# Kernel tuning notes

Measured on AMD Instinct MI355X. Metric: run time of the kernel, lower is better.

The kernel has to match this reference:

```python
import jax, jax.numpy as jnp
import numpy as np

EPS = 1e-7

def _dubbed_squash(v):
    norm = jnp.linalg.norm(v, axis=-1, keepdims=True)
    coef = 1.0 - 1.0 / (jnp.exp(norm) + EPS)
    return coef * v / (norm + EPS)

def setup_inputs() -> dict:
    key = jax.random.key(0)
    k1, k2, k3 = jax.random.split(key, 3)
    B, N, dp = 16, 1152, 8   # batch, num_primary_caps, dim_primary_caps
    D, dd = 10, 16           # num_digit_caps, dim_digit_caps
    primary_caps = jax.random.normal(k1, (B, N, dp), dtype=jnp.float32)
    W = jax.random.normal(k2, (D, N, dd, dp), dtype=jnp.float32) * 0.05
    B_prior = jax.random.normal(k3, (D, 1, N), dtype=jnp.float32) * 0.05
    return {"primary_caps": primary_caps, "W": W, "B_prior": B_prior}

def reference(primary_caps, W, B_prior):
    dp = primary_caps.shape[-1]
    # votes: U_hat[b,d,n,j] = W[d,n,j,i] @ u[b,n,i]   (replaces the tf.map_fn)
    U_hat = jnp.einsum('dnji,bni->bdnj', W, primary_caps)  # [B,D,N,dd]
    # self-similarity score matrix (as in original: full NxN matmul)
    A = jnp.einsum('bdnj,bdmj->bdnm', U_hat, U_hat) / jnp.sqrt(
        jnp.asarray(dp, dtype=primary_caps.dtype))          # [B,D,N,N]
    A_sum = jnp.sum(A, axis=2, keepdims=True)               # [B,D,1,N]
    C = jax.nn.softmax(A_sum, axis=1)                       # softmax over digit axis
    # weighted combine with learned log-priors: (B+C) @ U_hat -> [B,D,1,dd] -> squeeze
    S = jnp.einsum('bdkn,bdnj->bdj', B_prior[None] + C, U_hat)  # [B,D,dd]
    return _dubbed_squash(S)
```

## Files before the change

### kernel.cpp

```cpp
#include <hip/hip_runtime.h>

constexpr int BN = 16, NN = 1152, DP = 8, ND = 10, DD = 16;
constexpr int NBLK = BN * ND;
constexpr int GG = 64;
constexpr int KPT = NN / GG;
constexpr unsigned MAG1 = 0xC0FFEE01u;
constexpr int SPIN_CAP = 1 << 20;

__global__ __launch_bounds__(1024) void caps_one(
    const float* __restrict__ u, const float* __restrict__ W,
    const float* __restrict__ Bp, float* __restrict__ A,
    unsigned* __restrict__ flags, float* __restrict__ out)
{
    __shared__ float ul[NN * DP];
    __shared__ float bpl[NN];
    __shared__ float coeff[NN];
    __shared__ float Tpart[GG][17];
    __shared__ float Tl[16];
    __shared__ float Spart[GG][17];

    const int t = threadIdx.x;
    const int x = blockIdx.x;
    const int i = (x & 7) * 20 + (x >> 3);
    const int b = i & 15, d = i >> 4;
    const int j = t & 15, g = t >> 4;
    constexpr float RS8 = 0.35355339059327373f;

    {
        const float4* src = reinterpret_cast<const float4*>(u + (size_t)b * NN * DP);
        float4* dst4 = reinterpret_cast<float4*>(ul);
        for (int i2 = t; i2 < NN * DP / 4; i2 += 1024) dst4[i2] = src[i2];
        if (t < NN / 4)
            reinterpret_cast<float4*>(bpl)[t] =
                reinterpret_cast<const float4*>(Bp + (size_t)d * NN)[t];
    }
    __syncthreads();

    float uh[KPT];
    float tacc = 0.f;
    const float* Wd = W + (size_t)d * NN * DD * DP;
#pragma unroll 6
    for (int k = 0; k < KPT; ++k) {
        const int n = g + GG * k;
        const float4 w0 = *reinterpret_cast<const float4*>(
            Wd + ((size_t)n * DD + j) * DP);
        const float4 w1 = *reinterpret_cast<const float4*>(
            Wd + ((size_t)n * DD + j) * DP + 4);
        const float4 u0 = reinterpret_cast<const float4*>(ul)[n * 2];
        const float4 u1 = reinterpret_cast<const float4*>(ul)[n * 2 + 1];
        const float s = w0.x * u0.x + w0.y * u0.y + w0.z * u0.z + w0.w * u0.w
                      + w1.x * u1.x + w1.y * u1.y + w1.z * u1.z + w1.w * u1.w;
        uh[k] = s;
        tacc += s;
    }

    Tpart[g][j] = tacc;
    __syncthreads();
    if (t < 16) {
        float s = 0.f;
#pragma unroll
        for (int gg = 0; gg < GG; ++gg) s += Tpart[gg][t];
        Tl[t] = s;
    }
    __syncthreads();

    {
        float* Arow = A + (size_t)(b * ND + d) * NN;
        const float Tj = Tl[j];
#pragma unroll
        for (int k = 0; k < KPT; ++k) {
            float v = Tj * uh[k];
            v += __shfl_xor(v, 8, 16);
            v += __shfl_xor(v, 4, 16);
            v += __shfl_xor(v, 2, 16);
            v += __shfl_xor(v, 1, 16);
            if (j == 0) Arow[g + GG * k] = v * RS8;
        }
    }

    __syncthreads();
    if (t == 0) {
        asm volatile("buffer_wbl2 sc1\n\ts_waitcnt vmcnt(0)" ::: "memory");
        __hip_atomic_store(&flags[b * ND + d], MAG1, __ATOMIC_RELAXED,
                           __HIP_MEMORY_SCOPE_AGENT);
    }
    if (t < ND) {
        int spins = 0;
        while (__hip_atomic_load(&flags[b * ND + t], __ATOMIC_RELAXED,
                                 __HIP_MEMORY_SCOPE_AGENT) != MAG1) {
            __builtin_amdgcn_s_sleep(2);
            if (++spins > SPIN_CAP) break;
        }
        asm volatile("buffer_inv sc0 sc1\n\ts_waitcnt vmcnt(0)" ::: "memory");
    }
    asm volatile("" ::: "memory");
    __syncthreads();

    {
        const float* Ab = A + (size_t)b * ND * NN;
        if (t < NN / 2) {
            const int n0 = 2 * t;
            float a0[ND], a1[ND];
#pragma unroll
            for (int q = 0; q < ND; ++q) {
                const float2 p = *reinterpret_cast<const float2*>(
                    Ab + (size_t)q * NN + n0);
                a0[q] = p.x; a1[q] = p.y;
            }
            float m0 = a0[0], m1 = a1[0];
#pragma unroll
            for (int q = 1; q < ND; ++q) {
                m0 = fmaxf(m0, a0[q]); m1 = fmaxf(m1, a1[q]);
            }
            float se0 = 0.f, se1 = 0.f;
#pragma unroll
            for (int q = 0; q < ND; ++q) {
                a0[q] = expf(a0[q] - m0); se0 += a0[q];
                a1[q] = expf(a1[q] - m1); se1 += a1[q];
            }
            coeff[n0]     = bpl[n0]     + a0[d] / se0;
            coeff[n0 + 1] = bpl[n0 + 1] + a1[d] / se1;
        }
    }
    __syncthreads();

    float sacc = 0.f;
#pragma unroll
    for (int k = 0; k < KPT; ++k) sacc += coeff[g + GG * k] * uh[k];
    Spart[g][j] = sacc;
    __syncthreads();
    if (t < 16) {
        float Sv = 0.f;
#pragma unroll
        for (int gg = 0; gg < GG; ++gg) Sv += Spart[gg][t];
        float n2 = Sv * Sv;
#pragma unroll
        for (int off = 8; off >= 1; off >>= 1) n2 += __shfl_xor(n2, off, 16);
        const float nrm = sqrtf(n2);
        const float coef = 1.f - 1.f / (expf(nrm) + 1e-7f);
        out[((size_t)b * ND + d) * DD + t] = Sv * (coef / (nrm + 1e-7f));
    }
}

extern "C" void kernel_launch(void* const* d_in, const int* in_sizes, int n_in,
                              void* d_out, int out_size, void* d_ws, size_t ws_size,
                              hipStream_t stream) {
    const float* u  = nullptr;
    const float* W  = nullptr;
    const float* Bp = nullptr;
    for (int i = 0; i < n_in; ++i) {
        const int s = in_sizes[i];
        if (s == BN * NN * DP)            u  = (const float*)d_in[i];
        else if (s == ND * NN * DD * DP)  W  = (const float*)d_in[i];
        else if (s == ND * NN)            Bp = (const float*)d_in[i];
    }
    float* out = (float*)d_out;
    char*  wsc = (char*)d_ws;
    float*    A     = (float*)wsc;
    unsigned* flags = (unsigned*)(wsc + (1u << 20));

    caps_one<<<dim3(NBLK), 1024, 0, stream>>>(u, W, Bp, A, flags, out);
}
```

Before: 81.09 us.

## Split fused kernel into two launches instead of inter-block flag spin barrier

Replaces the single kernel's cross-block flag/spin synchronization with two kernel launches. The first computes votes and similarity sums, writing U_hat and A to workspace. The second reloads A into LDS, computes the softmax coefficients, and reads U_hat back from global memory. This removes the fragile spin-wait and its cache writeback and invalidate, but adds a launch boundary and about 11.8 MB of extra global traffic for U_hat.

New measurement: 83.00 us. 1.02x slower.

```diff
diff --git a/kernel.cpp b/kernel.cpp
--- a/kernel.cpp
+++ b/kernel.cpp
@@ -4,35 +4,28 @@
 constexpr int NBLK = BN * ND;
 constexpr int GG = 64;
 constexpr int KPT = NN / GG;
-constexpr unsigned MAG1 = 0xC0FFEE01u;
-constexpr int SPIN_CAP = 1 << 20;
+constexpr float RS8 = 0.35355339059327373f;
 
-__global__ __launch_bounds__(1024) void caps_one(
+__global__ __launch_bounds__(1024) void caps_k1(
     const float* __restrict__ u, const float* __restrict__ W,
-    const float* __restrict__ Bp, float* __restrict__ A,
-    unsigned* __restrict__ flags, float* __restrict__ out)
+    float* __restrict__ Uhat,
+    float* __restrict__ A)
 {
     __shared__ float ul[NN * DP];
-    __shared__ float bpl[NN];
-    __shared__ float coeff[NN];
     __shared__ float Tpart[GG][17];
     __shared__ float Tl[16];
-    __shared__ float Spart[GG][17];
+    __shared__ float Al[NN];
 
     const int t = threadIdx.x;
     const int x = blockIdx.x;
     const int i = (x & 7) * 20 + (x >> 3);
     const int b = i & 15, d = i >> 4;
     const int j = t & 15, g = t >> 4;
-    constexpr float RS8 = 0.35355339059327373f;
 
     {
         const float4* src = reinterpret_cast<const float4*>(u + (size_t)b * NN * DP);
         float4* dst4 = reinterpret_cast<float4*>(ul);
         for (int i2 = t; i2 < NN * DP / 4; i2 += 1024) dst4[i2] = src[i2];
-        if (t < NN / 4)
-            reinterpret_cast<float4*>(bpl)[t] =
-                reinterpret_cast<const float4*>(Bp + (size_t)d * NN)[t];
     }
     __syncthreads();
 
@@ -54,6 +47,13 @@
         tacc += s;
     }
 
+    {
+        float* Urow = Uhat + (size_t)(b * ND + d) * NN * DD;
+#pragma unroll
+        for (int k = 0; k < KPT; ++k)
+            Urow[(size_t)(g + GG * k) * DD + j] = uh[k];
+    }
+
     Tpart[g][j] = tacc;
     __syncthreads();
     if (t < 16) {
@@ -65,7 +65,6 @@
     __syncthreads();
 
     {
-        float* Arow = A + (size_t)(b * ND + d) * NN;
         const float Tj = Tl[j];
 #pragma unroll
         for (int k = 0; k < KPT; ++k) {
@@ -74,59 +73,70 @@
             v += __shfl_xor(v, 4, 16);
             v += __shfl_xor(v, 2, 16);
             v += __shfl_xor(v, 1, 16);
-            if (j == 0) Arow[g + GG * k] = v * RS8;
-        }
-    }
-
-    __syncthreads();
-    if (t == 0) {
-        asm volatile("buffer_wbl2 sc1\n\ts_waitcnt vmcnt(0)" ::: "memory");
-        __hip_atomic_store(&flags[b * ND + d], MAG1, __ATOMIC_RELAXED,
-                           __HIP_MEMORY_SCOPE_AGENT);
-    }
-    if (t < ND) {
-        int spins = 0;
-        while (__hip_atomic_load(&flags[b * ND + t], __ATOMIC_RELAXED,
-                                 __HIP_MEMORY_SCOPE_AGENT) != MAG1) {
-            __builtin_amdgcn_s_sleep(2);
-            if (++spins > SPIN_CAP) break;
-        }
-        asm volatile("buffer_inv sc0 sc1\n\ts_waitcnt vmcnt(0)" ::: "memory");
-    }
-    asm volatile("" ::: "memory");
-    __syncthreads();
-
-    {
-        const float* Ab = A + (size_t)b * ND * NN;
-        if (t < NN / 2) {
-            const int n0 = 2 * t;
-            float a0[ND], a1[ND];
-#pragma unroll
-            for (int q = 0; q < ND; ++q) {
-                const float2 p = *reinterpret_cast<const float2*>(
-                    Ab + (size_t)q * NN + n0);
-                a0[q] = p.x; a1[q] = p.y;
-            }
-            float m0 = a0[0], m1 = a1[0];
-#pragma unroll
-            for (int q = 1; q < ND; ++q) {
-                m0 = fmaxf(m0, a0[q]); m1 = fmaxf(m1, a1[q]);
-            }
-            float se0 = 0.f, se1 = 0.f;
-#pragma unroll
-            for (int q = 0; q < ND; ++q) {
-                a0[q] = expf(a0[q] - m0); se0 += a0[q];
-                a1[q] = expf(a1[q] - m1); se1 += a1[q];
-            }
-            coeff[n0]     = bpl[n0]     + a0[d] / se0;
-            coeff[n0 + 1] = bpl[n0 + 1] + a1[d] / se1;
+            if (j == 0) Al[g + GG * k] = v * RS8;
         }
     }
     __syncthreads();
+    if (t < NN / 4)
+        reinterpret_cast<float4*>(A + (size_t)(b * ND + d) * NN)[t] =
+            reinterpret_cast<const float4*>(Al)[t];
+}
 
+__global__ __launch_bounds__(1024) void caps_k2(
+    const float* __restrict__ Uhat, const float* __restrict__ A,
+    const float* __restrict__ Bp, float* __restrict__ out)
+{
+    __shared__ float Alds[ND * NN];
+    __shared__ float bpl[NN];
+    __shared__ float coeff[NN];
+    __shared__ float Spart[GG][17];
+
+    const int t = threadIdx.x;
+    const int x = blockIdx.x;
+    const int i = (x & 7) * 20 + (x >> 3);
+    const int b = i & 15, d = i >> 4;
+    const int j = t & 15, g = t >> 4;
+
+    {
+        const float4* Ab4 = reinterpret_cast<const float4*>(A + (size_t)b * ND * NN);
+        float4* dst4 = reinterpret_cast<float4*>(Alds);
+        for (int i2 = t; i2 < ND * NN / 4; i2 += 1024) dst4[i2] = Ab4[i2];
+        if (t < NN / 4)
+            reinterpret_cast<float4*>(bpl)[t] =
+                reinterpret_cast<const float4*>(Bp + (size_t)d * NN)[t];
+    }
+    __syncthreads();
+
+    if (t < NN / 2) {
+        const int n0 = 2 * t;
+        float a0[ND], a1[ND];
+#pragma unroll
+        for (int q = 0; q < ND; ++q) {
+            const float2 p = *reinterpret_cast<const float2*>(
+                Alds + q * NN + n0);
+            a0[q] = p.x; a1[q] = p.y;
+        }
+        float m0 = a0[0], m1 = a1[0];
+#pragma unroll
+        for (int q = 1; q < ND; ++q) {
+            m0 = fmaxf(m0, a0[q]); m1 = fmaxf(m1, a1[q]);
+        }
+        float se0 = 0.f, se1 = 0.f;
+#pragma unroll
+        for (int q = 0; q < ND; ++q) {
+            a0[q] = expf(a0[q] - m0); se0 += a0[q];
+            a1[q] = expf(a1[q] - m1); se1 += a1[q];
+        }
+        coeff[n0]     = bpl[n0]     + a0[d] / se0;
+        coeff[n0 + 1] = bpl[n0 + 1] + a1[d] / se1;
+    }
+    __syncthreads();
+
+    const float* Urow = Uhat + (size_t)(b * ND + d) * NN * DD;
     float sacc = 0.f;
 #pragma unroll
-    for (int k = 0; k < KPT; ++k) sacc += coeff[g + GG * k] * uh[k];
+    for (int k = 0; k < KPT; ++k)
+        sacc += coeff[g + GG * k] * Urow[(size_t)(g + GG * k) * DD + j];
     Spart[g][j] = sacc;
     __syncthreads();
     if (t < 16) {
@@ -156,8 +166,9 @@
     }
     float* out = (float*)d_out;
     char*  wsc = (char*)d_ws;
-    float*    A     = (float*)wsc;
-    unsigned* flags = (unsigned*)(wsc + (1u << 20));
+    float* Uhat = (float*)wsc;
+    float* A    = (float*)(wsc + (16u << 20));
 
-    caps_one<<<dim3(NBLK), 1024, 0, stream>>>(u, W, Bp, A, flags, out);
+    caps_k1<<<dim3(NBLK), 1024, 0, stream>>>(u, W, Uhat, A);
+    caps_k2<<<dim3(NBLK), 1024, 0, stream>>>(Uhat, A, Bp, out);
 }
```
